# Optimization experiments

Hardware: AMD Instinct MI355X
Metric: run time of the kernel (lower is better)

Reference implementation:

```python
import jax, jax.numpy as jnp
import numpy as np

# ConvTemporalGraphical (GRIP) forward, eval mode (Dropout = identity).
# All convs are 1x1, i.e. channel-mixing matmuls.

N, V, C_IN, C_OUT, K = 64, 256, 64, 64, 6


def setup_inputs() -> dict:
    key = jax.random.key(0)
    ks = jax.random.split(key, 11)
    x = jax.random.normal(ks[0], (N, C_OUT, V), dtype=jnp.float32)
    xo = jax.random.normal(ks[1], (N, C_IN, V), dtype=jnp.float32)
    A = jax.random.uniform(ks[2], (N, K, V, V), dtype=jnp.float32)
    s = 0.1
    w1 = jax.random.normal(ks[3], (16, 5), dtype=jnp.float32) * s
    b1 = jax.random.normal(ks[4], (16,), dtype=jnp.float32) * s
    w2 = jax.random.normal(ks[5], (32, 16), dtype=jnp.float32) * s
    b2 = jax.random.normal(ks[6], (32,), dtype=jnp.float32) * s
    w3 = jax.random.normal(ks[7], (64, 32), dtype=jnp.float32) * s
    b3 = jax.random.normal(ks[8], (64,), dtype=jnp.float32) * s
    wo = jax.random.normal(ks[9], (C_OUT, C_IN), dtype=jnp.float32) * s
    bo = jax.random.normal(ks[10], (C_OUT,), dtype=jnp.float32) * s
    return {"x": x, "xo": xo, "A": A, "w1": w1, "b1": b1, "w2": w2,
            "b2": b2, "w3": w3, "b3": b3, "wo": wo, "bo": bo}


def reference(x, xo, A, w1, b1, w2, b2, w3, b3, wo, bo):
    # convo: 1x1 Conv1d over channels -> [N, C_OUT, V]
    xo_c = jnp.einsum('niv,oi->nov', xo, wo) + bo[None, :, None]
    # adjmatder on A[:, :5]: 1x1 Conv2d stack 5->16->32->64 (Dropout is eval identity)
    h = jax.nn.relu(jnp.einsum('nivw,oi->novw', A[:, :5], w1) + b1[None, :, None, None])
    h = jax.nn.relu(jnp.einsum('nivw,oi->novw', h, w2) + b2[None, :, None, None])
    A_out = jax.nn.sigmoid(jnp.einsum('nivw,oi->novw', h, w3) + b3[None, :, None, None])
    # neighbor aggregation + sigmoid gating
    posterior_prob = jax.nn.sigmoid(jnp.einsum('ncv,ncvw->ncw', xo_c, A_out))
    return x * posterior_prob, A_out
```

## Files before the change

### kernel.cpp

```cpp
#include <hip/hip_runtime.h>
#include <hip/hip_bf16.h>

#define NV 256
#define NC 64
#define VW 65536
#define NE1 1048576
#define VB 32

typedef __attribute__((ext_vector_type(8))) short bf16x8;
typedef __attribute__((ext_vector_type(16))) float f32x16;
typedef __attribute__((ext_vector_type(2))) unsigned int uint2v;

union fu32 { float f; unsigned int u; };
union U4 { unsigned int u[4]; bf16x8 v8; };

static __device__ __forceinline__ short f2bf(float x) {
    union { __hip_bfloat16 b; short s; } u;
    u.b = __float2bfloat16(x);
    return u.s;
}
static __device__ __forceinline__ unsigned int cvt_pk_bf16(float a, float b) {
    unsigned int r;
    asm("v_cvt_pk_bf16_f32 %0, %1, %2" : "=v"(r) : "v"(a), "v"(b));
    return r;
}

__global__ __launch_bounds__(256) void k1_xoc(
    const float* __restrict__ xo, const float* __restrict__ wo,
    const float* __restrict__ bo, float* __restrict__ xoc)
{
    const int idx = blockIdx.x * 256 + threadIdx.x;
    const int v = idx & 255;
    const int c = (idx >> 8) & 63;
    const int n = idx >> 14;
    const float* xon = xo + (size_t)n * 64 * NV;
    const float* wrow = wo + c * 64;
    float s = bo[c];
#pragma unroll
    for (int i = 0; i < 64; ++i)
        s = fmaf(wrow[i], xon[i * NV + v], s);
    xoc[idx] = s;
}

template <bool USE_PART>
__global__ __launch_bounds__(256) void k2_mfma(
    const float* __restrict__ A,
    const float* __restrict__ w1, const float* __restrict__ b1,
    const float* __restrict__ w2, const float* __restrict__ b2,
    const float* __restrict__ w3, const float* __restrict__ b3,
    const float* __restrict__ xoc,
    float* __restrict__ Aout, float* __restrict__ gout)
{
    __shared__ float xocs[NC][VB];

    const int t    = threadIdx.x;
    const int wt   = t >> 6;
    const int lane = t & 63;
    const int lo   = lane & 31;
    const int hi   = lane >> 5;
    const int vbase = blockIdx.x * VB;
    const int n    = blockIdx.y;
    const int w0   = wt << 6;

    for (int e = t; e < NC * VB; e += 256) {
        const int c = e >> 5, j = e & (VB - 1);
        xocs[c][j] = xoc[(size_t)n * (NC * NV) + c * NV + vbase + j];
    }
    __syncthreads();

    bf16x8 af[2][2];
#pragma unroll
    for (int ct = 0; ct < 2; ++ct)
#pragma unroll
        for (int h = 0; h < 2; ++h) {
            const float* wp = w3 + ((ct << 5) + lo) * 32 + (h << 4) + (hi << 3);
            bf16x8 pk;
#pragma unroll
            for (int e = 0; e < 8; ++e) pk[e] = f2bf(wp[e]);
            af[ct][h] = pk;
        }
    bf16x8 af2;
#pragma unroll
    for (int e = 0; e < 8; ++e) af2[e] = f2bf(w2[lo * 16 + (hi << 3) + e]);

    float gacc[2][16][2];
#pragma unroll
    for (int ct = 0; ct < 2; ++ct)
#pragma unroll
        for (int r = 0; r < 16; ++r) {
            gacc[ct][r][0] = 0.0f;
            gacc[ct][r][1] = 0.0f;
        }

    const float* An  = A    + (size_t)n * 6 * VW;
    float*       Aon = Aout + (size_t)n * NC * VW;
    const float NLOG2E = -1.4426950408889634f;

    const float* ap0 = An + (size_t)vbase * NV + w0 + lane;
    float a0 = ap0[0], a1 = ap0[VW], a2 = ap0[2 * VW],
          a3 = ap0[3 * VW], a4 = ap0[4 * VW];

    for (int vi = 0; vi < VB; ++vi) {
        const int v = vbase + vi;

        const int vn = (vi + 1 < VB) ? (vi + 1) : vi;
        const float* apn = ap0 + (size_t)vn * NV;
        const float na0 = apn[0], na1 = apn[VW], na2 = apn[2 * VW],
                    na3 = apn[3 * VW], na4 = apn[4 * VW];

        unsigned int h1p[8];
#pragma unroll
        for (int m = 0; m < 8; ++m) {
            float sa = b1[2 * m];
            float sb = b1[2 * m + 1];
            sa = fmaf(w1[(2 * m) * 5 + 0], a0, sa);
            sa = fmaf(w1[(2 * m) * 5 + 1], a1, sa);
            sa = fmaf(w1[(2 * m) * 5 + 2], a2, sa);
            sa = fmaf(w1[(2 * m) * 5 + 3], a3, sa);
            sa = fmaf(w1[(2 * m) * 5 + 4], a4, sa);
            sb = fmaf(w1[(2 * m + 1) * 5 + 0], a0, sb);
            sb = fmaf(w1[(2 * m + 1) * 5 + 1], a1, sb);
            sb = fmaf(w1[(2 * m + 1) * 5 + 2], a2, sb);
            sb = fmaf(w1[(2 * m + 1) * 5 + 3], a3, sb);
            sb = fmaf(w1[(2 * m + 1) * 5 + 4], a4, sb);
            h1p[m] = cvt_pk_bf16(fmaxf(sa, 0.0f), fmaxf(sb, 0.0f));
        }

        U4 b1T0, b1T1;
#pragma unroll
        for (int j = 0; j < 4; ++j) {
            uint2v r = __builtin_amdgcn_permlane32_swap(h1p[j], h1p[4 + j],
                                                        false, false);
            b1T0.u[j] = r.x;
            b1T1.u[j] = r.y;
        }
        f32x16 d20, d21;
#pragma unroll
        for (int r = 0; r < 16; ++r) {
            const float bv = b2[(r & 3) + ((r >> 2) << 3) + (hi << 2)];
            d20[r] = bv; d21[r] = bv;
        }
        d20 = __builtin_amdgcn_mfma_f32_32x32x16_bf16(af2, b1T0.v8, d20, 0, 0, 0);
        d21 = __builtin_amdgcn_mfma_f32_32x32x16_bf16(af2, b1T1.v8, d21, 0, 0, 0);

        unsigned int p[8], q[8];
#pragma unroll
        for (int j = 0; j < 8; ++j) {
            p[j] = cvt_pk_bf16(fmaxf(d20[2 * j], 0.0f), fmaxf(d20[2 * j + 1], 0.0f));
            q[j] = cvt_pk_bf16(fmaxf(d21[2 * j], 0.0f), fmaxf(d21[2 * j + 1], 0.0f));
        }
        U4 b3f[2][2];
#pragma unroll
        for (int h = 0; h < 2; ++h) {
            uint2v r02 = __builtin_amdgcn_permlane32_swap(p[4 * h + 0], p[4 * h + 2], false, false);
            uint2v r13 = __builtin_amdgcn_permlane32_swap(p[4 * h + 1], p[4 * h + 3], false, false);
            b3f[0][h].u[0] = r02.x; b3f[0][h].u[2] = r02.y;
            b3f[0][h].u[1] = r13.x; b3f[0][h].u[3] = r13.y;
            uint2v s02 = __builtin_amdgcn_permlane32_swap(q[4 * h + 0], q[4 * h + 2], false, false);
            uint2v s13 = __builtin_amdgcn_permlane32_swap(q[4 * h + 1], q[4 * h + 3], false, false);
            b3f[1][h].u[0] = s02.x; b3f[1][h].u[2] = s02.y;
            b3f[1][h].u[1] = s13.x; b3f[1][h].u[3] = s13.y;
        }

        float* rowp = Aon + (size_t)v * NV + w0 + lane;

#pragma unroll
        for (int ct = 0; ct < 2; ++ct) {
            f32x16 d0, d1;
#pragma unroll
            for (int r = 0; r < 16; ++r) { d0[r] = 0.0f; d1[r] = 0.0f; }
            d0 = __builtin_amdgcn_mfma_f32_32x32x16_bf16(af[ct][0], b3f[0][0].v8, d0, 0, 0, 0);
            d0 = __builtin_amdgcn_mfma_f32_32x32x16_bf16(af[ct][1], b3f[0][1].v8, d0, 0, 0, 0);
            d1 = __builtin_amdgcn_mfma_f32_32x32x16_bf16(af[ct][0], b3f[1][0].v8, d1, 0, 0, 0);
            d1 = __builtin_amdgcn_mfma_f32_32x32x16_bf16(af[ct][1], b3f[1][1].v8, d1, 0, 0, 0);
#pragma unroll
            for (int r = 0; r < 16; ++r) {
                const int cx = (ct << 5) + (r & 3) + ((r >> 2) << 3);
                const int cy = cx + 4;
                fu32 ux, uy, mx, my;
                ux.f = d0[r]; uy.f = d1[r];
                uint2v m = __builtin_amdgcn_permlane32_swap(ux.u, uy.u, false, false);
                mx.u = m.x; my.u = m.y;
                const float vx = __builtin_amdgcn_rcpf(
                    1.0f + __builtin_amdgcn_exp2f(fmaf(mx.f, NLOG2E, b3[cx] * NLOG2E)));
                const float vy = __builtin_amdgcn_rcpf(
                    1.0f + __builtin_amdgcn_exp2f(fmaf(my.f, NLOG2E, b3[cy] * NLOG2E)));
                __builtin_nontemporal_store(vx, rowp + (size_t)cx * VW);
                __builtin_nontemporal_store(vy, rowp + (size_t)cy * VW);
                gacc[ct][r][0] = fmaf(xocs[cx][vi], vx, gacc[ct][r][0]);
                gacc[ct][r][1] = fmaf(xocs[cy][vi], vy, gacc[ct][r][1]);
            }
        }

        a0 = na0; a1 = na1; a2 = na2; a3 = na3; a4 = na4;
    }

    if (USE_PART) {
        float* gp = gout + (size_t)blockIdx.x * NE1
                         + (size_t)n * (NC * NV) + w0 + lane;
#pragma unroll
        for (int ct = 0; ct < 2; ++ct)
#pragma unroll
            for (int r = 0; r < 16; ++r) {
                const int cx = (ct << 5) + (r & 3) + ((r >> 2) << 3);
                gp[cx * NV]       = gacc[ct][r][0];
                gp[(cx + 4) * NV] = gacc[ct][r][1];
            }
    } else {
        float* pn = gout + (size_t)n * (NC * NV) + w0 + lane;
#pragma unroll
        for (int ct = 0; ct < 2; ++ct)
#pragma unroll
            for (int r = 0; r < 16; ++r) {
                const int cx = (ct << 5) + (r & 3) + ((r >> 2) << 3);
                atomicAdd(pn + cx * NV,       gacc[ct][r][0]);
                atomicAdd(pn + (cx + 4) * NV, gacc[ct][r][1]);
            }
    }
}

template <bool USE_PART>
__global__ __launch_bounds__(256) void k3_gate(
    const float* __restrict__ x, const float* __restrict__ g,
    float* __restrict__ out1)
{
    const int idx = blockIdx.x * 256 + threadIdx.x;
    float s;
    if (USE_PART) {
        s = g[idx];
#pragma unroll
        for (int b = 1; b < NV / VB; ++b)
            s += g[(size_t)b * NE1 + idx];
    } else {
        s = g[idx];
    }
    const float p = 1.0f / (1.0f + __expf(-s));
    out1[idx] = x[idx] * p;
}

extern "C" void kernel_launch(void* const* d_in, const int* in_sizes, int n_in,
                              void* d_out, int out_size, void* d_ws, size_t ws_size,
                              hipStream_t stream)
{
    const float* x  = (const float*)d_in[0];
    const float* xo = (const float*)d_in[1];
    const float* A  = (const float*)d_in[2];
    const float* w1 = (const float*)d_in[3];
    const float* b1 = (const float*)d_in[4];
    const float* w2 = (const float*)d_in[5];
    const float* b2 = (const float*)d_in[6];
    const float* w3 = (const float*)d_in[7];
    const float* b3 = (const float*)d_in[8];
    const float* wo = (const float*)d_in[9];
    const float* bo = (const float*)d_in[10];

    float* out1 = (float*)d_out;
    float* Aout = (float*)d_out + NE1;

    float* xoc  = (float*)d_ws;
    float* gbuf = (float*)d_ws + NE1;

    const bool use_part =
        ws_size >= (size_t)(NE1 + (NV / VB) * NE1) * sizeof(float);

    k1_xoc<<<NE1 / 256, 256, 0, stream>>>(xo, wo, bo, xoc);
    if (use_part) {
        k2_mfma<true><<<dim3(NV / VB, 64), 256, 0, stream>>>(
            A, w1, b1, w2, b2, w3, b3, xoc, Aout, gbuf);
        k3_gate<true><<<NE1 / 256, 256, 0, stream>>>(x, gbuf, out1);
    } else {
        hipMemsetAsync(gbuf, 0, (size_t)NE1 * sizeof(float), stream);
        k2_mfma<false><<<dim3(NV / VB, 64), 256, 0, stream>>>(
            A, w1, b1, w2, b2, w3, b3, xoc, Aout, gbuf);
        k3_gate<false><<<NE1 / 256, 256, 0, stream>>>(x, gbuf, out1);
    }
}
```

Measured before the change: 279.9 us.

## Stage sigmoid outputs in LDS for coalesced 16-byte Aout row stores

Each 64-channel by 256-column output slice per v is now written into a 64KB shared-memory staging buffer and then stored to global memory as 16-byte vector nontemporal stores over full rows. Before, each lane did scalar stores after a permlane swap. The bias is folded into the MFMA accumulator init, and the per-element permlane swap is removed by keeping the MFMA's native row mapping. The aim is wider, better-coalesced global writes to the large Aout tensor. The cost is two block-wide barriers per v iteration and 64KB of LDS, which cuts occupancy to about one or two blocks per CU.

```diff
diff --git a/kernel.cpp b/kernel.cpp
--- a/kernel.cpp
+++ b/kernel.cpp
@@ -9,9 +9,9 @@
 
 typedef __attribute__((ext_vector_type(8))) short bf16x8;
 typedef __attribute__((ext_vector_type(16))) float f32x16;
+typedef __attribute__((ext_vector_type(4))) float f32x4;
 typedef __attribute__((ext_vector_type(2))) unsigned int uint2v;
 
-union fu32 { float f; unsigned int u; };
 union U4 { unsigned int u[4]; bf16x8 v8; };
 
 static __device__ __forceinline__ short f2bf(float x) {
@@ -51,6 +51,7 @@
     const float* __restrict__ xoc,
     float* __restrict__ Aout, float* __restrict__ gout)
 {
+    __shared__ float stage[NC * NV];
     __shared__ float xocs[NC][VB];
 
     const int t    = threadIdx.x;
@@ -83,14 +84,20 @@
 #pragma unroll
     for (int e = 0; e < 8; ++e) af2[e] = f2bf(w2[lo * 16 + (hi << 3) + e]);
 
-    float gacc[2][16][2];
+    f32x16 dinit[2];
 #pragma unroll
     for (int ct = 0; ct < 2; ++ct)
 #pragma unroll
-        for (int r = 0; r < 16; ++r) {
-            gacc[ct][r][0] = 0.0f;
-            gacc[ct][r][1] = 0.0f;
-        }
+        for (int r = 0; r < 16; ++r)
+            dinit[ct][r] = b3[(ct << 5) + (r & 3) + ((r >> 2) << 3) + (hi << 2)];
+
+    float gacc[2][2][16];
+#pragma unroll
+    for (int ct = 0; ct < 2; ++ct)
+#pragma unroll
+        for (int T = 0; T < 2; ++T)
+#pragma unroll
+            for (int r = 0; r < 16; ++r) gacc[ct][T][r] = 0.0f;
 
     const float* An  = A    + (size_t)n * 6 * VW;
     float*       Aon = Aout + (size_t)n * NC * VW;
@@ -162,60 +169,63 @@
             b3f[1][h].u[1] = s13.x; b3f[1][h].u[3] = s13.y;
         }
 
-        float* rowp = Aon + (size_t)v * NV + w0 + lane;
-
 #pragma unroll
         for (int ct = 0; ct < 2; ++ct) {
-            f32x16 d0, d1;
-#pragma unroll
-            for (int r = 0; r < 16; ++r) { d0[r] = 0.0f; d1[r] = 0.0f; }
+            f32x16 d0 = dinit[ct], d1 = dinit[ct];
             d0 = __builtin_amdgcn_mfma_f32_32x32x16_bf16(af[ct][0], b3f[0][0].v8, d0, 0, 0, 0);
             d0 = __builtin_amdgcn_mfma_f32_32x32x16_bf16(af[ct][1], b3f[0][1].v8, d0, 0, 0, 0);
             d1 = __builtin_amdgcn_mfma_f32_32x32x16_bf16(af[ct][0], b3f[1][0].v8, d1, 0, 0, 0);
             d1 = __builtin_amdgcn_mfma_f32_32x32x16_bf16(af[ct][1], b3f[1][1].v8, d1, 0, 0, 0);
 #pragma unroll
             for (int r = 0; r < 16; ++r) {
-                const int cx = (ct << 5) + (r & 3) + ((r >> 2) << 3);
-                const int cy = cx + 4;
-                fu32 ux, uy, mx, my;
-                ux.f = d0[r]; uy.f = d1[r];
-                uint2v m = __builtin_amdgcn_permlane32_swap(ux.u, uy.u, false, false);
-                mx.u = m.x; my.u = m.y;
+                const int c = (ct << 5) + (r & 3) + ((r >> 2) << 3) + (hi << 2);
                 const float vx = __builtin_amdgcn_rcpf(
-                    1.0f + __builtin_amdgcn_exp2f(fmaf(mx.f, NLOG2E, b3[cx] * NLOG2E)));
+                    1.0f + __builtin_amdgcn_exp2f(d0[r] * NLOG2E));
                 const float vy = __builtin_amdgcn_rcpf(
-                    1.0f + __builtin_amdgcn_exp2f(fmaf(my.f, NLOG2E, b3[cy] * NLOG2E)));
-                __builtin_nontemporal_store(vx, rowp + (size_t)cx * VW);
-                __builtin_nontemporal_store(vy, rowp + (size_t)cy * VW);
-                gacc[ct][r][0] = fmaf(xocs[cx][vi], vx, gacc[ct][r][0]);
-                gacc[ct][r][1] = fmaf(xocs[cy][vi], vy, gacc[ct][r][1]);
+                    1.0f + __builtin_amdgcn_exp2f(d1[r] * NLOG2E));
+                stage[c * NV + w0 + lo]      = vx;
+                stage[c * NV + w0 + 32 + lo] = vy;
+                gacc[ct][0][r] = fmaf(xocs[c][vi], vx, gacc[ct][0][r]);
+                gacc[ct][1][r] = fmaf(xocs[c][vi], vy, gacc[ct][1][r]);
             }
         }
+        __syncthreads();
+
+#pragma unroll
+        for (int k = 0; k < 16; ++k) {
+            const int c = (k << 2) + wt;
+            const f32x4 val = *(const f32x4*)&stage[c * NV + (lane << 2)];
+            __builtin_nontemporal_store(
+                val, (f32x4*)(Aon + (size_t)c * VW + (size_t)v * NV + (lane << 2)));
+        }
+        __syncthreads();
 
         a0 = na0; a1 = na1; a2 = na2; a3 = na3; a4 = na4;
     }
 
     if (USE_PART) {
         float* gp = gout + (size_t)blockIdx.x * NE1
-                         + (size_t)n * (NC * NV) + w0 + lane;
+                         + (size_t)n * (NC * NV) + w0;
 #pragma unroll
         for (int ct = 0; ct < 2; ++ct)
 #pragma unroll
-            for (int r = 0; r < 16; ++r) {
-                const int cx = (ct << 5) + (r & 3) + ((r >> 2) << 3);
-                gp[cx * NV]       = gacc[ct][r][0];
-                gp[(cx + 4) * NV] = gacc[ct][r][1];
-            }
+            for (int T = 0; T < 2; ++T)
+#pragma unroll
+                for (int r = 0; r < 16; ++r) {
+                    const int c = (ct << 5) + (r & 3) + ((r >> 2) << 3) + (hi << 2);
+                    gp[c * NV + (T << 5) + lo] = gacc[ct][T][r];
+                }
     } else {
-        float* pn = gout + (size_t)n * (NC * NV) + w0 + lane;
+        float* pn = gout + (size_t)n * (NC * NV) + w0;
 #pragma unroll
         for (int ct = 0; ct < 2; ++ct)
 #pragma unroll
-            for (int r = 0; r < 16; ++r) {
-                const int cx = (ct << 5) + (r & 3) + ((r >> 2) << 3);
-                atomicAdd(pn + cx * NV,       gacc[ct][r][0]);
-                atomicAdd(pn + (cx + 4) * NV, gacc[ct][r][1]);
-            }
+            for (int T = 0; T < 2; ++T)
+#pragma unroll
+                for (int r = 0; r < 16; ++r) {
+                    const int c = (ct << 5) + (r & 3) + ((r >> 2) << 3) + (hi << 2);
+                    atomicAdd(pn + c * NV + (T << 5) + lo, gacc[ct][T][r]);
+                }
     }
 }
 
```

Measured after the change: 263.1 us. -6.0%, faster.
